# Optimization experiments

Hardware: AMD Instinct MI355X
Metric: run time of the kernel (lower is better)

## Reference

```python
import jax, jax.numpy as jnp
import numpy as np


def setup_inputs() -> dict:
    key = jax.random.key(0)
    x = jax.random.normal(key, (8, 64, 64, 64), dtype=jnp.float32)
    return {"x": x}


def reference(x) -> jnp.ndarray:
    b, c, h, w = x.shape
    hw = h * w
    # channel-mean "joint" map: [b, hw]
    avg = jnp.mean(x, axis=1).reshape(b, hw)
    # scores[b, i, j] = avg[b, i] * avg[b, j]  (rank-1 outer product, hw x hw)
    scores = avg[:, :, None] * avg[:, None, :]
    attn = jax.nn.softmax(scores, axis=-1)  # [b, hw, hw]
    V = x.reshape(b, c, hw)
    # out[b,c,n] = sum_m V[b,c,m] * attn[b,n,m]  (== bmm(V, attn^T))
    out = jnp.einsum('bcm,bnm->bcn', V, attn)
    return out.reshape(b, c, h, w)
```

## Files before the change

kernel.cpp:

```cpp
#include <hip/hip_runtime.h>


constexpr int B = 8;
constexpr int C = 64;
constexpr int HW = 4096;
constexpr int K = 14;
constexpr int CHUNK = 128;
constexpr int NCHUNK = HW / CHUNK;
constexpr int NROWS = C + 1;

__device__ __constant__ float c_invfact[K] = {
    1.0f, 1.0f, 5.0e-1f,
    1.6666666666666666e-1f, 4.1666666666666664e-2f, 8.3333333333333332e-3f,
    1.3888888888888889e-3f, 1.9841269841269841e-4f, 2.4801587301587302e-5f,
    2.7557319223985893e-6f, 2.7557319223985888e-7f, 2.5052108385441720e-8f,
    2.0876756987868100e-9f, 1.6059043836821613e-10f,
};

__global__ __launch_bounds__(512) void saam_pass1(const float* __restrict__ x,
                                                  float* __restrict__ avg,
                                                  float* __restrict__ part) {
    __shared__ float tile[CHUNK][C + 1];
    __shared__ float partial[8][C][K];
    __shared__ float colsum[2][CHUNK];
    __shared__ float amem[CHUNK];
    __shared__ float zred[2][K];

    const int t = threadIdx.x;
    const int b = blockIdx.x >> 5;
    const int chunk = blockIdx.x & 31;
    const int m0 = chunk * CHUNK;

    {
        const int col4 = t & 31;
        const int rbase = t >> 5;
#pragma unroll
        for (int it = 0; it < 4; ++it) {
            const int row = it * 16 + rbase;
            const float4 v = *reinterpret_cast<const float4*>(
                x + (size_t)(b * C + row) * HW + m0 + col4 * 4);
            const int m = col4 * 4;
            tile[m + 0][row] = v.x;
            tile[m + 1][row] = v.y;
            tile[m + 2][row] = v.z;
            tile[m + 3][row] = v.w;
        }
    }
    __syncthreads();

    if (t < 256) {
        const int g = t >> 7, m = t & 127;
        float s = 0.f;
#pragma unroll
        for (int j = 0; j < 32; ++j) s += tile[m][g * 32 + j];
        colsum[g][m] = s;
    }
    __syncthreads();

    if (t < CHUNK) {
        const int m = t;
        const float a = (colsum[0][m] + colsum[1][m]) * (1.0f / 64.0f);
        amem[m] = a;
        avg[b * HW + m0 + m] = a;
        float pw[K];
        float p = a;
#pragma unroll
        for (int k = 0; k < K; ++k) { pw[k] = p; p *= a; }
#pragma unroll
        for (int k = 0; k < K; ++k) {
            float v = pw[k];
#pragma unroll
            for (int off = 32; off > 0; off >>= 1) v += __shfl_down(v, off, 64);
            pw[k] = v;
        }
        if ((t & 63) == 0) {
            const int w = t >> 6;
#pragma unroll
            for (int k = 0; k < K; ++k) zred[w][k] = pw[k];
        }
    }
    __syncthreads();

    {
        const int s = t >> 6, c = t & 63;
        float acc[K];
#pragma unroll
        for (int k = 0; k < K; ++k) acc[k] = 0.f;
        const int mb = s * 16;
#pragma unroll
        for (int j = 0; j < 16; ++j) {
            const int m = mb + j;
            const float a = amem[m];
            float p = tile[m][c];
#pragma unroll
            for (int k = 0; k < K; ++k) { acc[k] += p; p *= a; }
        }
#pragma unroll
        for (int k = 0; k < K; ++k) partial[s][c][k] = acc[k];
    }
    __syncthreads();

    float* dst = part + (size_t)(b * NCHUNK + chunk) * NROWS * K;
    for (int idx = t; idx < NROWS * K; idx += 512) {
        const int cc = idx / K, k = idx - cc * K;
        float s;
        if (cc < C) {
            s = 0.f;
#pragma unroll
            for (int w = 0; w < 8; ++w) s += partial[w][cc][k];
        } else {
            s = (k == 0) ? (float)CHUNK : (zred[0][k - 1] + zred[1][k - 1]);
        }
        dst[idx] = s;
    }
}

__global__ __launch_bounds__(256) void saam_pass2(const float* __restrict__ avg,
                                                  const float* __restrict__ part,
                                                  float* __restrict__ out) {
    __shared__ float coef[2][K];
    const int t = threadIdx.x;
    const int bc = blockIdx.x >> 2;
    const int q = blockIdx.x & 3;
    const int b = bc >> 6;
    const int c = bc & 63;
    const int n0 = q * 1024;

    if (t < 2 * K) {
        const int row = t / K;
        const int k = t - row * K;
        const int cc = row ? C : c;
        const float* p = part + (size_t)b * NCHUNK * NROWS * K + cc * K + k;
        float s = 0.f;
#pragma unroll
        for (int ch = 0; ch < NCHUNK; ++ch) s += p[(size_t)ch * NROWS * K];
        coef[row][k] = s * c_invfact[k];
    }
    __syncthreads();

    float cf0[K], cf1[K];
#pragma unroll
    for (int k = 0; k < K; ++k) { cf0[k] = coef[0][k]; cf1[k] = coef[1][k]; }

    const float4 tv = *reinterpret_cast<const float4*>(avg + b * HW + n0 + t * 4);

    auto evalone = [&](float tt) {
        float num = cf0[K - 1];
        float den = cf1[K - 1];
#pragma unroll
        for (int k = K - 2; k >= 0; --k) {
            num = __builtin_fmaf(num, tt, cf0[k]);
            den = __builtin_fmaf(den, tt, cf1[k]);
        }
        return num / den;
    };

    float4 o;
    o.x = evalone(tv.x);
    o.y = evalone(tv.y);
    o.z = evalone(tv.z);
    o.w = evalone(tv.w);

    *reinterpret_cast<float4*>(out + (size_t)(b * C + c) * HW + n0 + t * 4) = o;
}

extern "C" void kernel_launch(void* const* d_in, const int* in_sizes, int n_in,
                              void* d_out, int out_size, void* d_ws, size_t ws_size,
                              hipStream_t stream) {
    const float* x = (const float*)d_in[0];
    float* out = (float*)d_out;

    float* avg = (float*)d_ws;
    float* part = avg + (size_t)B * HW;

    saam_pass1<<<B * NCHUNK, 512, 0, stream>>>(x, avg, part);
    saam_pass2<<<B * C * HW / 1024, 256, 0, stream>>>(avg, part, out);
}
```

Measured before the change: 16.16 us.

## Restructure pass2 per spatial chunk with shared denominators and transposed partials

The partial-sum layout is transposed so each coefficient's per-chunk values are contiguous and can be reduced with float4 loads. Pass2 now uses one block per (batch, 128-position chunk) handling all 64 channels. It computes the denominator polynomial once per position as a reciprocal and reuses it across channels instead of dividing in every (b,c) block. Pass1's column sum also uses all 512 threads. The trade-off is fewer, larger pass2 blocks (256), each doing more serial work, and an approximate reciprocal in place of an exact division.

```diff
diff --git a/kernel.cpp b/kernel.cpp
--- a/kernel.cpp
+++ b/kernel.cpp
@@ -22,7 +22,7 @@
                                                   float* __restrict__ part) {
     __shared__ float tile[CHUNK][C + 1];
     __shared__ float partial[8][C][K];
-    __shared__ float colsum[2][CHUNK];
+    __shared__ float colsum[4][CHUNK];
     __shared__ float amem[CHUNK];
     __shared__ float zred[2][K];
 
@@ -48,18 +48,19 @@
     }
     __syncthreads();
 
-    if (t < 256) {
+    {
         const int g = t >> 7, m = t & 127;
         float s = 0.f;
 #pragma unroll
-        for (int j = 0; j < 32; ++j) s += tile[m][g * 32 + j];
+        for (int j = 0; j < 16; ++j) s += tile[m][g * 16 + j];
         colsum[g][m] = s;
     }
     __syncthreads();
 
     if (t < CHUNK) {
         const int m = t;
-        const float a = (colsum[0][m] + colsum[1][m]) * (1.0f / 64.0f);
+        const float a = (colsum[0][m] + colsum[1][m] + colsum[2][m] + colsum[3][m])
+                        * (1.0f / 64.0f);
         amem[m] = a;
         avg[b * HW + m0 + m] = a;
         float pw[K];
@@ -100,7 +101,6 @@
     }
     __syncthreads();
 
-    float* dst = part + (size_t)(b * NCHUNK + chunk) * NROWS * K;
     for (int idx = t; idx < NROWS * K; idx += 512) {
         const int cc = idx / K, k = idx - cc * K;
         float s;
@@ -111,57 +111,79 @@
         } else {
             s = (k == 0) ? (float)CHUNK : (zred[0][k - 1] + zred[1][k - 1]);
         }
-        dst[idx] = s;
+        part[((size_t)(b * NROWS + cc) * K + k) * NCHUNK + chunk] = s;
     }
 }
 
-__global__ __launch_bounds__(256) void saam_pass2(const float* __restrict__ avg,
+__global__ __launch_bounds__(512) void saam_pass2(const float* __restrict__ avg,
                                                   const float* __restrict__ part,
                                                   float* __restrict__ out) {
-    __shared__ float coef[2][K];
+    __shared__ float coef[NROWS][K];
+    __shared__ float amem[CHUNK];
+    __shared__ float rden[CHUNK];
+
     const int t = threadIdx.x;
-    const int bc = blockIdx.x >> 2;
-    const int q = blockIdx.x & 3;
-    const int b = bc >> 6;
-    const int c = bc & 63;
-    const int n0 = q * 1024;
-
-    if (t < 2 * K) {
-        const int row = t / K;
-        const int k = t - row * K;
-        const int cc = row ? C : c;
-        const float* p = part + (size_t)b * NCHUNK * NROWS * K + cc * K + k;
-        float s = 0.f;
-#pragma unroll
-        for (int ch = 0; ch < NCHUNK; ++ch) s += p[(size_t)ch * NROWS * K];
-        coef[row][k] = s * c_invfact[k];
-    }
-    __syncthreads();
-
-    float cf0[K], cf1[K];
-#pragma unroll
-    for (int k = 0; k < K; ++k) { cf0[k] = coef[0][k]; cf1[k] = coef[1][k]; }
-
-    const float4 tv = *reinterpret_cast<const float4*>(avg + b * HW + n0 + t * 4);
-
-    auto evalone = [&](float tt) {
-        float num = cf0[K - 1];
-        float den = cf1[K - 1];
+    const int b = blockIdx.x >> 5;
+    const int n0 = (blockIdx.x & 31) * CHUNK;
+
+    for (int idx = t; idx < NROWS * K; idx += 512) {
+        const int cc = idx / K, k = idx - cc * K;
+        const float4* p = reinterpret_cast<const float4*>(
+            part + ((size_t)(b * NROWS + cc) * K + k) * NCHUNK);
+        float4 s0 = p[0], s1 = p[1], s2 = p[2], s3 = p[3];
+        float4 s4 = p[4], s5 = p[5], s6 = p[6], s7 = p[7];
+        float s = ((s0.x + s0.y) + (s0.z + s0.w)) + ((s1.x + s1.y) + (s1.z + s1.w))
+                + ((s2.x + s2.y) + (s2.z + s2.w)) + ((s3.x + s3.y) + (s3.z + s3.w))
+                + ((s4.x + s4.y) + (s4.z + s4.w)) + ((s5.x + s5.y) + (s5.z + s5.w))
+                + ((s6.x + s6.y) + (s6.z + s6.w)) + ((s7.x + s7.y) + (s7.z + s7.w));
+        coef[cc][k] = s * c_invfact[k];
+    }
+    if (t < 32) {
+        const float4 v = *reinterpret_cast<const float4*>(avg + b * HW + n0 + t * 4);
+        amem[t * 4 + 0] = v.x;
+        amem[t * 4 + 1] = v.y;
+        amem[t * 4 + 2] = v.z;
+        amem[t * 4 + 3] = v.w;
+    }
+    __syncthreads();
+
+    if (t < CHUNK) {
+        const float tt = amem[t];
+        float den = coef[C][K - 1];
+#pragma unroll
+        for (int k = K - 2; k >= 0; --k) den = __builtin_fmaf(den, tt, coef[C][k]);
+        rden[t] = __builtin_amdgcn_rcpf(den);
+    }
+    __syncthreads();
+
+    const int qid = t & 31, cg = t >> 5;
+    float tt[4], rd[4];
+#pragma unroll
+    for (int j = 0; j < 4; ++j) {
+        tt[j] = amem[qid * 4 + j];
+        rd[j] = rden[qid * 4 + j];
+    }
+#pragma unroll
+    for (int j = 0; j < 4; ++j) {
+        const int c = cg * 4 + j;
+        float cf[K];
+#pragma unroll
+        for (int k = 0; k < K; ++k) cf[k] = coef[c][k];
+        float4 o;
+        float n0v = cf[K - 1], n1v = cf[K - 1], n2v = cf[K - 1], n3v = cf[K - 1];
 #pragma unroll
         for (int k = K - 2; k >= 0; --k) {
-            num = __builtin_fmaf(num, tt, cf0[k]);
-            den = __builtin_fmaf(den, tt, cf1[k]);
-        }
-        return num / den;
-    };
-
-    float4 o;
-    o.x = evalone(tv.x);
-    o.y = evalone(tv.y);
-    o.z = evalone(tv.z);
-    o.w = evalone(tv.w);
-
-    *reinterpret_cast<float4*>(out + (size_t)(b * C + c) * HW + n0 + t * 4) = o;
+            n0v = __builtin_fmaf(n0v, tt[0], cf[k]);
+            n1v = __builtin_fmaf(n1v, tt[1], cf[k]);
+            n2v = __builtin_fmaf(n2v, tt[2], cf[k]);
+            n3v = __builtin_fmaf(n3v, tt[3], cf[k]);
+        }
+        o.x = n0v * rd[0];
+        o.y = n1v * rd[1];
+        o.z = n2v * rd[2];
+        o.w = n3v * rd[3];
+        *reinterpret_cast<float4*>(out + (size_t)(b * C + c) * HW + n0 + qid * 4) = o;
+    }
 }
 
 extern "C" void kernel_launch(void* const* d_in, const int* in_sizes, int n_in,
@@ -174,5 +196,5 @@
     float* part = avg + (size_t)B * HW;
 
     saam_pass1<<<B * NCHUNK, 512, 0, stream>>>(x, avg, part);
-    saam_pass2<<<B * C * HW / 1024, 256, 0, stream>>>(avg, part, out);
+    saam_pass2<<<B * NCHUNK, 512, 0, stream>>>(avg, part, out);
 }
```

New measurement: 19.52 us. 20.8% more time.
